# Performance work log

Measured on AMD Instinct MI355X. Metric: run time of the kernel, lower is better.

Reference implementation:

```python
import jax, jax.numpy as jnp
import numpy as np

N_P, N_A, N_S, D = 50000, 25000, 1, 64
ALPHA = 0.2  # leaky_relu negative slope
E_P2P, E_P2A, E_A2P, E_A2A = 800000, 400000, 400000, 400000


def _gat(z_msg, wh_dst, aw, src, dst, n_dst):
    """Per-edge-type GAT: score = leaky_relu(attn_fc([z_src ; Wh_dst])),
    segment softmax over destination, weighted scatter-sum of z_src.
    Attention linear is split into src/dst halves and applied per-node (cheaper)."""
    d = z_msg.shape[1]
    e = (z_msg @ aw[:d])[src] + (wh_dst @ aw[d:])[dst]  # [E]
    e = jnp.where(e > 0, e, ALPHA * e)                   # leaky_relu
    m = jax.ops.segment_max(e, dst, num_segments=n_dst)
    ex = jnp.exp(e - m[dst])
    den = jax.ops.segment_sum(ex, dst, num_segments=n_dst)
    w = ex / den[dst]                                    # per-dst softmax (mailbox softmax)
    return jax.ops.segment_sum(w[:, None] * z_msg[src], dst, num_segments=n_dst)


def setup_inputs() -> dict:
    ks = jax.random.split(jax.random.key(0), 32)
    sc = 1.0 / np.sqrt(D)
    f32, i32 = jnp.float32, jnp.int32
    inp = {
        "feat_P": jax.random.normal(ks[0], (N_P, D), f32),
        "feat_A": jax.random.normal(ks[1], (N_A, D), f32),
        "feat_state": jax.random.normal(ks[2], (N_S, D), f32),
    }
    for i, n in enumerate(["P", "A", "p2p", "p2a", "a2p", "a2a", "p2s", "a2s", "in"]):
        inp["W_" + n] = jax.random.normal(ks[3 + i], (D, D), f32) * sc
        inp["b_" + n] = jnp.zeros((D,), f32)
    for i, n in enumerate(["p2p", "p2a", "a2p", "a2a", "p2s", "a2s"]):
        inp["a_" + n] = jax.random.normal(ks[12 + i], (2 * D,), f32) * sc
    inp["src_p2p"] = jax.random.randint(ks[18], (E_P2P,), 0, N_P, i32)
    inp["dst_p2p"] = jax.random.randint(ks[19], (E_P2P,), 0, N_P, i32)
    inp["src_p2a"] = jax.random.randint(ks[20], (E_P2A,), 0, N_P, i32)
    inp["dst_p2a"] = jax.random.randint(ks[21], (E_P2A,), 0, N_A, i32)
    inp["src_a2p"] = jax.random.randint(ks[22], (E_A2P,), 0, N_A, i32)
    inp["dst_a2p"] = jax.random.randint(ks[23], (E_A2P,), 0, N_P, i32)
    inp["src_a2a"] = jax.random.randint(ks[24], (E_A2A,), 0, N_A, i32)
    inp["dst_a2a"] = jax.random.randint(ks[25], (E_A2A,), 0, N_A, i32)
    inp["src_p2s"] = jnp.arange(N_P, dtype=i32)
    inp["dst_p2s"] = jnp.zeros((N_P,), i32)
    inp["src_a2s"] = jnp.arange(N_A, dtype=i32)
    inp["dst_a2s"] = jnp.zeros((N_A,), i32)
    return inp


def reference(feat_P, feat_A, feat_state,
              W_P, b_P, W_A, b_A, W_p2p, b_p2p, W_p2a, b_p2a, W_a2p, b_a2p,
              W_a2a, b_a2a, W_p2s, b_p2s, W_a2s, b_a2s, W_in, b_in,
              a_p2p, a_p2a, a_a2p, a_a2a, a_p2s, a_a2s,
              src_p2p, dst_p2p, src_p2a, dst_p2a, src_a2p, dst_a2p,
              src_a2a, dst_a2a, src_p2s, dst_p2s, src_a2s, dst_a2s):
    Wh_P = feat_P @ W_P + b_P          # self transform per node type
    Wh_A = feat_A @ W_A + b_A
    Wh_in = feat_state @ W_in + b_in   # 'in' self-loop message to state
    h_P = jax.nn.relu(
        Wh_P
        + _gat(feat_P @ W_p2p + b_p2p, Wh_P, a_p2p, src_p2p, dst_p2p, N_P)
        + _gat(feat_A @ W_a2p + b_a2p, Wh_P, a_a2p, src_a2p, dst_a2p, N_P))
    h_A = jax.nn.relu(
        Wh_A
        + _gat(feat_P @ W_p2a + b_p2a, Wh_A, a_p2a, src_p2a, dst_p2a, N_A)
        + _gat(feat_A @ W_a2a + b_a2a, Wh_A, a_a2a, src_a2a, dst_a2a, N_A))
    h_S = jax.nn.relu(
        Wh_in
        + _gat(feat_P @ W_p2s + b_p2s, Wh_in, a_p2s, src_p2s, dst_p2s, N_S)
        + _gat(feat_A @ W_a2s + b_a2s, Wh_in, a_a2s, src_a2s, dst_a2s, N_S))
    return (h_P, h_A, h_S)
```

## Files before the change

kernel.cpp:

```cpp
#include <hip/hip_runtime.h>
#include <math.h>

#define ALPHA 0.2f
#define NP 50000
#define NA 25000
#define NBINS 150000
#define ABASE 100000
#define NBUCK 586
#define CH 4096
#define CAP 8192
#define GP ((NP + 63) / 64)
#define GA ((NA + 63) / 64)
#define SB_P 384
#define SB_A 192

typedef unsigned short u16;
typedef __attribute__((ext_vector_type(8))) short bf16x8;
typedef __attribute__((ext_vector_type(8))) unsigned short u16x8;
typedef __attribute__((ext_vector_type(4))) float f32x4;

__device__ __forceinline__ float bf2f(u16 u) { return __uint_as_float(((unsigned)u) << 16); }
__device__ __forceinline__ u16 f2bf(float f) {
    unsigned x = __float_as_uint(f);
    return (u16)((x + 0x7fffu + ((x >> 16) & 1u)) >> 16);
}

struct K1Args {
    const int *s0, *d0, *s1, *d1, *s2, *d2, *s3, *d3;
    int E0, E1, E2, E3, Etot, nblk;
    int *cursor0, *ebuf;
    const float *feat_P, *feat_A, *feat_S;
    const float *W_p2s, *b_p2s, *a_p2s, *W_a2s, *b_a2s, *a_a2s, *W_in, *b_in;
    float *numP, *numA, *den2;
};

struct K2Args {
    const int *ebuf; const int *cursor0;
    int *ssrc; int *offs;
    const float *feat_P, *feat_A, *feat_S;
    const float *W_P, *b_P, *W_A, *b_A, *W_p2p, *b_p2p, *W_p2a, *b_p2a,
                *W_a2p, *b_a2p, *W_a2a, *b_a2a, *W_p2s, *b_p2s, *W_a2s, *b_a2s,
                *W_in, *b_in;
    const float *a_p2p, *a_p2a, *a_a2p, *a_a2a;
    float *WhP, *WhA;
    u16 *z_p2p, *z_p2a, *z_a2p, *z_a2a;
    float *ss_p2p, *sd_p2p, *ss_p2a, *sd_p2a, *ss_a2p, *sd_a2p, *ss_a2a, *sd_a2a;
    const float *numP, *numA, *den2;
    float *outS;
};

__device__ __forceinline__ void edge_decode(int k,
    const int* __restrict__ s0, const int* __restrict__ d0, int E0,
    const int* __restrict__ s1, const int* __restrict__ d1, int E1,
    const int* __restrict__ s2, const int* __restrict__ d2, int E2,
    const int* __restrict__ s3, const int* __restrict__ d3,
    int& src, int& bin) {
    if (k < E0) { src = s0[k]; bin = 2 * d0[k]; return; }
    k -= E0; if (k < E1) { src = s1[k]; bin = 2 * d1[k] + 1; return; }
    k -= E1; if (k < E2) { src = s2[k]; bin = ABASE + 2 * d2[k]; return; }
    k -= E2; src = s3[k]; bin = ABASE + 2 * d3[k] + 1;
}

__global__ __launch_bounds__(256) void k1_kernel(K1Args A) {
    __shared__ int h[NBUCK];
    __shared__ int base[NBUCK];
    int bid = blockIdx.x;
    int tid = threadIdx.x;
    if (bid < A.nblk) {
        for (int i = tid; i < NBUCK; i += 256) h[i] = 0;
        __syncthreads();
        int b0 = bid * CH;
        int b1 = min(b0 + CH, A.Etot);
        int cbin[16], csrc[16];
#pragma unroll
        for (int it = 0; it < 16; ++it) {
            int i = b0 + it * 256 + tid;
            int bin = -1, src = 0;
            if (i < b1)
                edge_decode(i, A.s0, A.d0, A.E0, A.s1, A.d1, A.E1,
                            A.s2, A.d2, A.E2, A.s3, A.d3, src, bin);
            cbin[it] = bin; csrc[it] = src;
            if (bin >= 0) atomicAdd(&h[bin >> 8], 1);
        }
        __syncthreads();
        for (int i = tid; i < NBUCK; i += 256) {
            int c = h[i];
            base[i] = c ? (i * CAP + atomicAdd(&A.cursor0[i], c)) : 0;
            h[i] = 0;
        }
        __syncthreads();
#pragma unroll
        for (int it = 0; it < 16; ++it) {
            int bin = cbin[it];
            if (bin >= 0) {
                int bk = bin >> 8;
                int pos = base[bk] + atomicAdd(&h[bk], 1);
                if (pos < (bk + 1) * CAP)
                    A.ebuf[pos] = csrc[it] | ((bin & 255) << 16);
            }
        }
        return;
    }
    float* red = (float*)h;
    int sb = bid - A.nblk;
    bool isP = sb < SB_P;
    int bidl = isP ? sb : sb - SB_P;
    int nb = isP ? SB_P : SB_A;
    int N = isP ? NP : NA;
    const float* X   = isP ? A.feat_P : A.feat_A;
    const float* W   = isP ? A.W_p2s  : A.W_a2s;
    const float* b   = isP ? A.b_p2s  : A.b_a2s;
    const float* a   = isP ? A.a_p2s  : A.a_a2s;
    float* num       = isP ? A.numP   : A.numA;
    float* den       = isP ? &A.den2[0] : &A.den2[1];
    int lane = tid & 63, wv = tid >> 6;
    float v = 0.f;
    for (int c = 0; c < 64; ++c) v = fmaf(W[lane * 64 + c], a[c], v);
    float t0 = b[lane] * a[lane];
    float whc = A.b_in[lane];
    for (int k = 0; k < 64; ++k) whc = fmaf(A.feat_S[k], A.W_in[k * 64 + lane], whc);
    float t1 = whc * a[64 + lane];
#pragma unroll
    for (int o = 1; o < 64; o <<= 1) {
        t0 += __shfl_xor(t0, o, 64);
        t1 += __shfl_xor(t1, o, 64);
    }
    float cbias = t0 + t1;
    float accx = 0.f, accd = 0.f;
    int gw = bidl * 4 + wv, waves = nb * 4;
    for (int r = gw; r < N; r += waves) {
        float x = X[(long long)r * 64 + lane];
        float ss = x * v;
#pragma unroll
        for (int o = 1; o < 64; o <<= 1) ss += __shfl_xor(ss, o, 64);
        float e = ss + cbias;
        e = e > 0.f ? e : ALPHA * e;
        float w = __expf(e);
        accx = fmaf(w, x, accx);
        accd += w;
    }
    red[wv * 64 + lane] = accx;
    if (lane == 0) red[256 + wv] = accd;
    __syncthreads();
    if (tid < 64) {
        float t = red[tid] + red[64 + tid] + red[128 + tid] + red[192 + tid];
        atomicAdd(&num[tid], t);
    }
    if (tid == 64) atomicAdd(den, red[256] + red[257] + red[258] + red[259]);
}

__device__ void scan_counts(const int* __restrict__ counts, int* sstart) {
    __shared__ int wtot_sb[4];
    int tid = threadIdx.x, lane = tid & 63, wv = tid >> 6;
    int carry = 0;
    for (int c = 0; c < 3; ++c) {
        int i = c * 256 + tid;
        int v = (i < NBUCK) ? min(counts[i], CAP) : 0;
        int x = v;
#pragma unroll
        for (int o = 1; o < 64; o <<= 1) {
            int y = __shfl_up(x, o, 64);
            if (lane >= o) x += y;
        }
        if (lane == 63) wtot_sb[wv] = x;
        __syncthreads();
        int woff = carry;
        for (int j = 0; j < wv; ++j) woff += wtot_sb[j];
        int ctot = wtot_sb[0] + wtot_sb[1] + wtot_sb[2] + wtot_sb[3];
        if (i < NBUCK) sstart[i] = x + woff - v;
        __syncthreads();
        carry += ctot;
    }
    if (tid == 0) sstart[NBUCK] = carry;
    __syncthreads();
}

__device__ __forceinline__ void xform_body3(int bid,
    const float* __restrict__ X, int N,
    const float* __restrict__ W0, const float* __restrict__ b0, float* __restrict__ Wh,
    const float* __restrict__ dA, float* __restrict__ sdA,
    const float* __restrict__ dB, float* __restrict__ sdB,
    const float* __restrict__ W1, const float* __restrict__ b1, u16* __restrict__ z1,
    const float* __restrict__ v1, float* __restrict__ s1,
    const float* __restrict__ W2, const float* __restrict__ b2, u16* __restrict__ z2,
    const float* __restrict__ v2, float* __restrict__ s2)
{
    int tid = threadIdx.x, wv = tid >> 6, lane = tid & 63;
    if (wv == 3) return;
    int g = lane >> 4, li = lane & 15;
    const float* Wm = wv == 0 ? W0 : wv == 1 ? W1 : W2;
    const float* bm = wv == 0 ? b0 : wv == 1 ? b1 : b2;
    const float* dv = wv == 0 ? dA : wv == 1 ? v1 : v2;
    float* sm       = wv == 0 ? sdA : wv == 1 ? s1 : s2;
    u16* zm         = wv == 1 ? z1 : wv == 2 ? z2 : nullptr;

    bf16x8 Bf[4][2];
#pragma unroll
    for (int cb = 0; cb < 4; ++cb)
#pragma unroll
        for (int kc = 0; kc < 2; ++kc) {
            bf16x8 t;
#pragma unroll
            for (int j = 0; j < 8; ++j)
                t[j] = (short)f2bf(Wm[(kc * 32 + g * 8 + j) * 64 + cb * 16 + li]);
            Bf[cb][kc] = t;
        }
    float bl[4], dvl[4], dbl[4];
#pragma unroll
    for (int cb = 0; cb < 4; ++cb) {
        bl[cb]  = bm[cb * 16 + li];
        dvl[cb] = dv[cb * 16 + li];
        dbl[cb] = (wv == 0) ? dB[cb * 16 + li] : 0.f;
    }
    int base0 = bid * 64;
#pragma unroll
    for (int rt = 0; rt < 4; ++rt) {
        int rbase = base0 + rt * 16;
        if (rbase >= N) break;
        int rowC = min(rbase + li, N - 1);
        bf16x8 Af[2];
#pragma unroll
        for (int kc = 0; kc < 2; ++kc) {
            const float* xp = X + (long long)rowC * 64 + kc * 32 + g * 8;
            float4 x0 = *(const float4*)xp;
            float4 x1 = *(const float4*)(xp + 4);
            bf16x8 t;
            t[0] = (short)f2bf(x0.x); t[1] = (short)f2bf(x0.y);
            t[2] = (short)f2bf(x0.z); t[3] = (short)f2bf(x0.w);
            t[4] = (short)f2bf(x1.x); t[5] = (short)f2bf(x1.y);
            t[6] = (short)f2bf(x1.z); t[7] = (short)f2bf(x1.w);
            Af[kc] = t;
        }
        f32x4 acc[4] = {{0,0,0,0},{0,0,0,0},{0,0,0,0},{0,0,0,0}};
#pragma unroll
        for (int kc = 0; kc < 2; ++kc)
#pragma unroll
            for (int cb = 0; cb < 4; ++cb)
                acc[cb] = __builtin_amdgcn_mfma_f32_16x16x32_bf16(Af[kc], Bf[cb][kc], acc[cb], 0, 0, 0);
        float pd[4] = {0,0,0,0}, pb[4] = {0,0,0,0};
#pragma unroll
        for (int cb = 0; cb < 4; ++cb)
#pragma unroll
            for (int r = 0; r < 4; ++r) {
                float val = acc[cb][r] + bl[cb];
                acc[cb][r] = val;
                pd[r] = fmaf(val, dvl[cb], pd[r]);
                pb[r] = fmaf(val, dbl[cb], pb[r]);
            }
#pragma unroll
        for (int o = 1; o < 16; o <<= 1)
#pragma unroll
            for (int r = 0; r < 4; ++r) {
                pd[r] += __shfl_xor(pd[r], o, 64);
                pb[r] += __shfl_xor(pb[r], o, 64);
            }
        int rg = rbase + g * 4;
        if (li == 0) {
#pragma unroll
            for (int r = 0; r < 4; ++r) {
                int row = rg + r;
                if (row < N) {
                    sm[row] = pd[r];
                    if (wv == 0) sdB[row] = pb[r];
                }
            }
        }
        if (wv == 0) {
#pragma unroll
            for (int r = 0; r < 4; ++r) {
                int row = rg + r;
                if (row < N)
#pragma unroll
                    for (int cb = 0; cb < 4; ++cb)
                        Wh[(long long)row * 64 + cb * 16 + li] = acc[cb][r];
            }
        } else {
#pragma unroll
            for (int r = 0; r < 4; ++r) {
                int row = rg + r;
                if (row < N)
#pragma unroll
                    for (int cb = 0; cb < 4; ++cb)
                        zm[(long long)row * 64 + cb * 16 + li] = f2bf(acc[cb][r]);
            }
        }
    }
}

__global__ __launch_bounds__(256) void k2_kernel(K2Args A) {
    __shared__ int smem_i[NBUCK + 1 + 768 + 4];
    __shared__ u16 lsrc[CAP];
    int bid = blockIdx.x;
    int tid = threadIdx.x, lane = tid & 63, wv = tid >> 6;
    if (bid < NBUCK) {
        int* sstart = smem_i;
        int* lcnt = smem_i + NBUCK + 1;
        int* loff = lcnt + 256;
        int* lcur = loff + 256;
        int* wtot = lcur + 256;
        int b = bid;
        scan_counts(A.cursor0, sstart);
        int pstart = sstart[b];
        int rstart = b * CAP;
        int cnt = min(A.cursor0[b], CAP);
        lcnt[tid] = 0;
        __syncthreads();
        for (int e = tid; e < cnt; e += 256)
            atomicAdd(&lcnt[((unsigned)A.ebuf[rstart + e]) >> 16], 1);
        __syncthreads();
        int v = lcnt[tid];
        int x = v;
#pragma unroll
        for (int o = 1; o < 64; o <<= 1) {
            int y = __shfl_up(x, o, 64);
            if (lane >= o) x += y;
        }
        if (lane == 63) wtot[wv] = x;
        __syncthreads();
        int woff = 0;
        for (int j = 0; j < wv; ++j) woff += wtot[j];
        int excl = x + woff - v;
        loff[tid] = excl;
        lcur[tid] = excl;
        __syncthreads();
        for (int e = tid; e < cnt; e += 256) {
            int val = A.ebuf[rstart + e];
            int pos = atomicAdd(&lcur[((unsigned)val) >> 16], 1);
            lsrc[pos] = (u16)(val & 0xFFFF);
        }
        __syncthreads();
        for (int i = tid; i < cnt; i += 256) A.ssrc[pstart + i] = (int)lsrc[i];
        int gb = b * 256 + tid;
        if (gb < NBINS) A.offs[gb] = pstart + loff[tid];
        if (b == 0 && tid == 0) A.offs[NBINS] = sstart[NBUCK];
        return;
    }
    bid -= NBUCK;
    if (bid < GP) {
        xform_body3(bid, A.feat_P, NP,
                    A.W_P, A.b_P, A.WhP, A.a_p2p + 64, A.sd_p2p, A.a_a2p + 64, A.sd_a2p,
                    A.W_p2p, A.b_p2p, A.z_p2p, A.a_p2p, A.ss_p2p,
                    A.W_p2a, A.b_p2a, A.z_p2a, A.a_p2a, A.ss_p2a);
        return;
    }
    bid -= GP;
    if (bid < GA) {
        xform_body3(bid, A.feat_A, NA,
                    A.W_A, A.b_A, A.WhA, A.a_p2a + 64, A.sd_p2a, A.a_a2a + 64, A.sd_a2a,
                    A.W_a2p, A.b_a2p, A.z_a2p, A.a_a2p, A.ss_a2p,
                    A.W_a2a, A.b_a2a, A.z_a2a, A.a_a2a, A.ss_a2a);
        return;
    }
    if (tid < 64) {
        int c = tid;
        float whc = A.b_in[c];
        for (int k = 0; k < 64; ++k) whc = fmaf(A.feat_S[k], A.W_in[k * 64 + c], whc);
        float mp = 0.f, ma = 0.f;
        for (int k = 0; k < 64; ++k) {
            mp = fmaf(A.numP[k], A.W_p2s[k * 64 + c], mp);
            ma = fmaf(A.numA[k], A.W_a2s[k * 64 + c], ma);
        }
        float r = whc + mp / A.den2[0] + A.b_p2s[c] + ma / A.den2[1] + A.b_a2s[c];
        A.outS[c] = fmaxf(r, 0.f);
    }
}

__device__ __forceinline__ void seg_gat_g8(const int* __restrict__ ssrc, int s0, int s1,
                                           const float* __restrict__ ss, float sd,
                                           const u16* __restrict__ z, int lane,
                                           float* __restrict__ acc) {
    int cnt = s1 - s0;
    if (cnt <= 0) return;
    int egrp = lane >> 3, cg8 = (lane & 7) * 8;
    if (cnt <= 64) {
        int s = 0; float w = 0.f;
        if (lane < cnt) {
            s = ssrc[s0 + lane];
            float e = ss[s] + sd;
            e = e > 0.f ? e : ALPHA * e;
            w = __expf(e);
        }
        float den = w;
#pragma unroll
        for (int o = 32; o > 0; o >>= 1) den += __shfl_xor(den, o, 64);
        w *= 1.f / den;
        int nit = (cnt + 7) >> 3;
        for (int it = 0; it < nit; ++it) {
            int ei = it * 8 + egrp;
            float wt = __shfl(w, ei, 64);
            int   st = __shfl(s, ei, 64);
            u16x8 q = *(const u16x8*)(z + (long long)st * 64 + cg8);
#pragma unroll
            for (int j = 0; j < 8; ++j)
                acc[j] = fmaf(wt, bf2f(q[j]), acc[j]);
        }
    } else {
        float den = 0.f;
        for (int i = s0 + lane; i < s1; i += 64) {
            float e = ss[ssrc[i]] + sd; e = e > 0.f ? e : ALPHA * e; den += __expf(e);
        }
#pragma unroll
        for (int o = 32; o > 0; o >>= 1) den += __shfl_xor(den, o, 64);
        float inv = 1.f / den;
        for (int c = s0; c < s1; c += 64) {
            int i = c + lane; int s = 0; float w = 0.f;
            if (i < s1) {
                s = ssrc[i];
                float e = ss[s] + sd; e = e > 0.f ? e : ALPHA * e;
                w = __expf(e) * inv;
            }
            int cc = min(64, s1 - c);
            int nit = (cc + 7) >> 3;
            for (int it = 0; it < nit; ++it) {
                int ei = it * 8 + egrp;
                float wt = __shfl(w, ei, 64);
                int   st = __shfl(s, ei, 64);
                u16x8 q = *(const u16x8*)(z + (long long)st * 64 + cg8);
#pragma unroll
                for (int j = 0; j < 8; ++j)
                    acc[j] = fmaf(wt, bf2f(q[j]), acc[j]);
            }
        }
    }
}

__global__ __launch_bounds__(256) void gat_all(
    const int* __restrict__ ssrc, const int* __restrict__ offs,
    const float* __restrict__ WhP, float* __restrict__ outP,
    const float* __restrict__ WhA, float* __restrict__ outA,
    const float* __restrict__ ss_p2p, const float* __restrict__ sd_p2p, const u16* __restrict__ z_p2p,
    const float* __restrict__ ss_a2p, const float* __restrict__ sd_a2p, const u16* __restrict__ z_a2p,
    const float* __restrict__ ss_p2a, const float* __restrict__ sd_p2a, const u16* __restrict__ z_p2a,
    const float* __restrict__ ss_a2a, const float* __restrict__ sd_a2a, const u16* __restrict__ z_a2a) {
    int lane = threadIdx.x & 63;
    int g = (blockIdx.x * blockDim.x + threadIdx.x) >> 6;
    if (g >= NP + NA) return;
    bool isP = g < NP;
    int d = isP ? g : g - NP;
    int bin0 = isP ? 2 * d : ABASE + 2 * d;
    int e0 = offs[bin0], e1 = offs[bin0 + 1], e2 = offs[bin0 + 2];
    float acc[8] = {0.f, 0.f, 0.f, 0.f, 0.f, 0.f, 0.f, 0.f};
    if (isP) {
        seg_gat_g8(ssrc, e0, e1, ss_p2p, sd_p2p[d], z_p2p, lane, acc);
        seg_gat_g8(ssrc, e1, e2, ss_a2p, sd_a2p[d], z_a2p, lane, acc);
    } else {
        seg_gat_g8(ssrc, e0, e1, ss_p2a, sd_p2a[d], z_p2a, lane, acc);
        seg_gat_g8(ssrc, e1, e2, ss_a2a, sd_a2a[d], z_a2a, lane, acc);
    }
#pragma unroll
    for (int o = 8; o <= 32; o <<= 1)
#pragma unroll
        for (int j = 0; j < 8; ++j)
            acc[j] += __shfl_xor(acc[j], o, 64);
    if (lane < 8) {
        const float* Wh = isP ? WhP : WhA;
        float* outp = isP ? outP : outA;
        const float* sp = &Wh[(long long)d * 64 + lane * 8];
        float4 s0v = *(const float4*)sp;
        float4 s1v = *(const float4*)(sp + 4);
        float4 r0, r1;
        r0.x = fmaxf(s0v.x + acc[0], 0.f); r0.y = fmaxf(s0v.y + acc[1], 0.f);
        r0.z = fmaxf(s0v.z + acc[2], 0.f); r0.w = fmaxf(s0v.w + acc[3], 0.f);
        r1.x = fmaxf(s1v.x + acc[4], 0.f); r1.y = fmaxf(s1v.y + acc[5], 0.f);
        r1.z = fmaxf(s1v.z + acc[6], 0.f); r1.w = fmaxf(s1v.w + acc[7], 0.f);
        float* op = &outp[(long long)d * 64 + lane * 8];
        *(float4*)op = r0;
        *(float4*)(op + 4) = r1;
    }
}

extern "C" void kernel_launch(void* const* d_in, const int* in_sizes, int n_in,
                              void* d_out, int out_size, void* d_ws, size_t ws_size,
                              hipStream_t stream) {
    const float* feat_P = (const float*)d_in[0];
    const float* feat_A = (const float*)d_in[1];
    const float* feat_S = (const float*)d_in[2];
    const float* W_P   = (const float*)d_in[3];  const float* b_P   = (const float*)d_in[4];
    const float* W_A   = (const float*)d_in[5];  const float* b_A   = (const float*)d_in[6];
    const float* W_p2p = (const float*)d_in[7];  const float* b_p2p = (const float*)d_in[8];
    const float* W_p2a = (const float*)d_in[9];  const float* b_p2a = (const float*)d_in[10];
    const float* W_a2p = (const float*)d_in[11]; const float* b_a2p = (const float*)d_in[12];
    const float* W_a2a = (const float*)d_in[13]; const float* b_a2a = (const float*)d_in[14];
    const float* W_p2s = (const float*)d_in[15]; const float* b_p2s = (const float*)d_in[16];
    const float* W_a2s = (const float*)d_in[17]; const float* b_a2s = (const float*)d_in[18];
    const float* W_in  = (const float*)d_in[19]; const float* b_in  = (const float*)d_in[20];
    const float* a_p2p = (const float*)d_in[21];
    const float* a_p2a = (const float*)d_in[22];
    const float* a_a2p = (const float*)d_in[23];
    const float* a_a2a = (const float*)d_in[24];
    const float* a_p2s = (const float*)d_in[25];
    const float* a_a2s = (const float*)d_in[26];
    const int* src_p2p = (const int*)d_in[27]; const int* dst_p2p = (const int*)d_in[28];
    const int* src_p2a = (const int*)d_in[29]; const int* dst_p2a = (const int*)d_in[30];
    const int* src_a2p = (const int*)d_in[31]; const int* dst_a2p = (const int*)d_in[32];
    const int* src_a2a = (const int*)d_in[33]; const int* dst_a2a = (const int*)d_in[34];
    int E_p2p = in_sizes[27], E_p2a = in_sizes[29], E_a2p = in_sizes[31], E_a2a = in_sizes[33];
    int E_tot = E_p2p + E_a2p + E_p2a + E_a2a;

    float* out = (float*)d_out;
    float* outP = out;
    float* outA = out + (long long)NP * 64;
    float* outS = out + (long long)(NP + NA) * 64;

    float* ws = (float*)d_ws;
    float* WhP = ws; ws += (long long)NP * 64;
    float* WhA = ws; ws += (long long)NA * 64;
    u16* z_p2p = (u16*)ws; ws += (long long)NP * 32;
    u16* z_p2a = (u16*)ws; ws += (long long)NP * 32;
    u16* z_a2p = (u16*)ws; ws += (long long)NA * 32;
    u16* z_a2a = (u16*)ws; ws += (long long)NA * 32;
    float* ss_p2p = ws; ws += NP;  float* sd_p2p = ws; ws += NP;
    float* ss_p2a = ws; ws += NP;  float* sd_p2a = ws; ws += NA;
    float* ss_a2p = ws; ws += NA;  float* sd_a2p = ws; ws += NP;
    float* ss_a2a = ws; ws += NA;  float* sd_a2a = ws; ws += NA;
    float* zreg = ws;
    int*   cursor0 = (int*)ws; ws += NBUCK;
    float* den2 = ws; ws += 2;
    float* numP = ws; ws += 64;
    float* numA = ws; ws += 64;
    size_t zbytes = (size_t)((char*)ws - (char*)zreg);
    int* iw = (int*)ws;
    int* ebuf = iw; iw += NBUCK * CAP;
    int* ssrc = iw; iw += E_tot;
    int* offs = iw; iw += NBINS + 1;

    const int T = 256;
    int nblk = (E_tot + CH - 1) / CH;

    hipMemsetAsync(zreg, 0, zbytes, stream);

    K1Args K1;
    K1.s0 = src_p2p; K1.d0 = dst_p2p; K1.s1 = src_a2p; K1.d1 = dst_a2p;
    K1.s2 = src_p2a; K1.d2 = dst_p2a; K1.s3 = src_a2a; K1.d3 = dst_a2a;
    K1.E0 = E_p2p; K1.E1 = E_a2p; K1.E2 = E_p2a; K1.E3 = E_a2a;
    K1.Etot = E_tot; K1.nblk = nblk;
    K1.cursor0 = cursor0; K1.ebuf = ebuf;
    K1.feat_P = feat_P; K1.feat_A = feat_A; K1.feat_S = feat_S;
    K1.W_p2s = W_p2s; K1.b_p2s = b_p2s; K1.a_p2s = a_p2s;
    K1.W_a2s = W_a2s; K1.b_a2s = b_a2s; K1.a_a2s = a_a2s;
    K1.W_in = W_in; K1.b_in = b_in;
    K1.numP = numP; K1.numA = numA; K1.den2 = den2;
    k1_kernel<<<nblk + SB_P + SB_A, T, 0, stream>>>(K1);

    K2Args K2;
    K2.ebuf = ebuf; K2.cursor0 = cursor0; K2.ssrc = ssrc; K2.offs = offs;
    K2.feat_P = feat_P; K2.feat_A = feat_A; K2.feat_S = feat_S;
    K2.W_P = W_P; K2.b_P = b_P; K2.W_A = W_A; K2.b_A = b_A;
    K2.W_p2p = W_p2p; K2.b_p2p = b_p2p; K2.W_p2a = W_p2a; K2.b_p2a = b_p2a;
    K2.W_a2p = W_a2p; K2.b_a2p = b_a2p; K2.W_a2a = W_a2a; K2.b_a2a = b_a2a;
    K2.W_p2s = W_p2s; K2.b_p2s = b_p2s; K2.W_a2s = W_a2s; K2.b_a2s = b_a2s;
    K2.W_in = W_in; K2.b_in = b_in;
    K2.a_p2p = a_p2p; K2.a_p2a = a_p2a; K2.a_a2p = a_a2p; K2.a_a2a = a_a2a;
    K2.WhP = WhP; K2.WhA = WhA;
    K2.z_p2p = z_p2p; K2.z_p2a = z_p2a; K2.z_a2p = z_a2p; K2.z_a2a = z_a2a;
    K2.ss_p2p = ss_p2p; K2.sd_p2p = sd_p2p; K2.ss_p2a = ss_p2a; K2.sd_p2a = sd_p2a;
    K2.ss_a2p = ss_a2p; K2.sd_a2p = sd_a2p; K2.ss_a2a = ss_a2a; K2.sd_a2a = sd_a2a;
    K2.numP = numP; K2.numA = numA; K2.den2 = den2; K2.outS = outS;
    k2_kernel<<<NBUCK + GP + GA + 1, T, 0, stream>>>(K2);

    gat_all<<<((NP + NA) * 64 + T - 1) / T, T, 0, stream>>>(ssrc, offs,
        WhP, outP, WhA, outA,
        ss_p2p, sd_p2p, z_p2p, ss_a2p, sd_a2p, z_a2p,
        ss_p2a, sd_p2a, z_p2a, ss_a2a, sd_a2a, z_a2a);
}
```

Baseline: 131.6 us.

## Move node transforms into the edge-bucketing kernel and store sorted sources as u16

The per-node MFMA transforms (Wh, z, and the attention src/dst scores) move out of k2 and into k1, where they run alongside the edge bucketing and state-reduction blocks. Each wave now handles one (matrix, row-block) item, so the previously idle fourth wave of every block does work, and k2 keeps only the sort/scan and the state output. The sorted source index array is narrowed from int to u16, which halves its write and read traffic in k2 and gat_all. The cost is a larger, more varied k1 grid. The u16 sources rely on node indices being below 65536.

```diff
diff --git a/kernel.cpp b/kernel.cpp
--- a/kernel.cpp
+++ b/kernel.cpp
@@ -11,6 +11,9 @@
 #define CAP 8192
 #define GP ((NP + 63) / 64)
 #define GA ((NA + 63) / 64)
+#define XWI_P (3 * GP)
+#define XWI (3 * GP + 3 * GA)
+#define XWB ((XWI + 3) / 4)
 #define SB_P 384
 #define SB_A 192
 
@@ -30,21 +33,21 @@
     int E0, E1, E2, E3, Etot, nblk;
     int *cursor0, *ebuf;
     const float *feat_P, *feat_A, *feat_S;
-    const float *W_p2s, *b_p2s, *a_p2s, *W_a2s, *b_a2s, *a_a2s, *W_in, *b_in;
-    float *numP, *numA, *den2;
-};
-
-struct K2Args {
-    const int *ebuf; const int *cursor0;
-    int *ssrc; int *offs;
-    const float *feat_P, *feat_A, *feat_S;
     const float *W_P, *b_P, *W_A, *b_A, *W_p2p, *b_p2p, *W_p2a, *b_p2a,
-                *W_a2p, *b_a2p, *W_a2a, *b_a2a, *W_p2s, *b_p2s, *W_a2s, *b_a2s,
-                *W_in, *b_in;
+                *W_a2p, *b_a2p, *W_a2a, *b_a2a;
     const float *a_p2p, *a_p2a, *a_a2p, *a_a2a;
     float *WhP, *WhA;
     u16 *z_p2p, *z_p2a, *z_a2p, *z_a2a;
     float *ss_p2p, *sd_p2p, *ss_p2a, *sd_p2a, *ss_a2p, *sd_a2p, *ss_a2a, *sd_a2a;
+    const float *W_p2s, *b_p2s, *a_p2s, *W_a2s, *b_a2s, *a_a2s, *W_in, *b_in;
+    float *numP, *numA, *den2;
+};
+
+struct K2Args {
+    const int *ebuf; const int *cursor0;
+    u16 *ssrc; int *offs;
+    const float *feat_S;
+    const float *W_p2s, *b_p2s, *W_a2s, *b_a2s, *W_in, *b_in;
     const float *numP, *numA, *den2;
     float *outS;
 };
@@ -61,139 +64,15 @@
     k -= E2; src = s3[k]; bin = ABASE + 2 * d3[k] + 1;
 }
 
-__global__ __launch_bounds__(256) void k1_kernel(K1Args A) {
-    __shared__ int h[NBUCK];
-    __shared__ int base[NBUCK];
-    int bid = blockIdx.x;
-    int tid = threadIdx.x;
-    if (bid < A.nblk) {
-        for (int i = tid; i < NBUCK; i += 256) h[i] = 0;
-        __syncthreads();
-        int b0 = bid * CH;
-        int b1 = min(b0 + CH, A.Etot);
-        int cbin[16], csrc[16];
-#pragma unroll
-        for (int it = 0; it < 16; ++it) {
-            int i = b0 + it * 256 + tid;
-            int bin = -1, src = 0;
-            if (i < b1)
-                edge_decode(i, A.s0, A.d0, A.E0, A.s1, A.d1, A.E1,
-                            A.s2, A.d2, A.E2, A.s3, A.d3, src, bin);
-            cbin[it] = bin; csrc[it] = src;
-            if (bin >= 0) atomicAdd(&h[bin >> 8], 1);
-        }
-        __syncthreads();
-        for (int i = tid; i < NBUCK; i += 256) {
-            int c = h[i];
-            base[i] = c ? (i * CAP + atomicAdd(&A.cursor0[i], c)) : 0;
-            h[i] = 0;
-        }
-        __syncthreads();
-#pragma unroll
-        for (int it = 0; it < 16; ++it) {
-            int bin = cbin[it];
-            if (bin >= 0) {
-                int bk = bin >> 8;
-                int pos = base[bk] + atomicAdd(&h[bk], 1);
-                if (pos < (bk + 1) * CAP)
-                    A.ebuf[pos] = csrc[it] | ((bin & 255) << 16);
-            }
-        }
-        return;
-    }
-    float* red = (float*)h;
-    int sb = bid - A.nblk;
-    bool isP = sb < SB_P;
-    int bidl = isP ? sb : sb - SB_P;
-    int nb = isP ? SB_P : SB_A;
-    int N = isP ? NP : NA;
-    const float* X   = isP ? A.feat_P : A.feat_A;
-    const float* W   = isP ? A.W_p2s  : A.W_a2s;
-    const float* b   = isP ? A.b_p2s  : A.b_a2s;
-    const float* a   = isP ? A.a_p2s  : A.a_a2s;
-    float* num       = isP ? A.numP   : A.numA;
-    float* den       = isP ? &A.den2[0] : &A.den2[1];
-    int lane = tid & 63, wv = tid >> 6;
-    float v = 0.f;
-    for (int c = 0; c < 64; ++c) v = fmaf(W[lane * 64 + c], a[c], v);
-    float t0 = b[lane] * a[lane];
-    float whc = A.b_in[lane];
-    for (int k = 0; k < 64; ++k) whc = fmaf(A.feat_S[k], A.W_in[k * 64 + lane], whc);
-    float t1 = whc * a[64 + lane];
-#pragma unroll
-    for (int o = 1; o < 64; o <<= 1) {
-        t0 += __shfl_xor(t0, o, 64);
-        t1 += __shfl_xor(t1, o, 64);
-    }
-    float cbias = t0 + t1;
-    float accx = 0.f, accd = 0.f;
-    int gw = bidl * 4 + wv, waves = nb * 4;
-    for (int r = gw; r < N; r += waves) {
-        float x = X[(long long)r * 64 + lane];
-        float ss = x * v;
-#pragma unroll
-        for (int o = 1; o < 64; o <<= 1) ss += __shfl_xor(ss, o, 64);
-        float e = ss + cbias;
-        e = e > 0.f ? e : ALPHA * e;
-        float w = __expf(e);
-        accx = fmaf(w, x, accx);
-        accd += w;
-    }
-    red[wv * 64 + lane] = accx;
-    if (lane == 0) red[256 + wv] = accd;
-    __syncthreads();
-    if (tid < 64) {
-        float t = red[tid] + red[64 + tid] + red[128 + tid] + red[192 + tid];
-        atomicAdd(&num[tid], t);
-    }
-    if (tid == 64) atomicAdd(den, red[256] + red[257] + red[258] + red[259]);
-}
-
-__device__ void scan_counts(const int* __restrict__ counts, int* sstart) {
-    __shared__ int wtot_sb[4];
-    int tid = threadIdx.x, lane = tid & 63, wv = tid >> 6;
-    int carry = 0;
-    for (int c = 0; c < 3; ++c) {
-        int i = c * 256 + tid;
-        int v = (i < NBUCK) ? min(counts[i], CAP) : 0;
-        int x = v;
-#pragma unroll
-        for (int o = 1; o < 64; o <<= 1) {
-            int y = __shfl_up(x, o, 64);
-            if (lane >= o) x += y;
-        }
-        if (lane == 63) wtot_sb[wv] = x;
-        __syncthreads();
-        int woff = carry;
-        for (int j = 0; j < wv; ++j) woff += wtot_sb[j];
-        int ctot = wtot_sb[0] + wtot_sb[1] + wtot_sb[2] + wtot_sb[3];
-        if (i < NBUCK) sstart[i] = x + woff - v;
-        __syncthreads();
-        carry += ctot;
-    }
-    if (tid == 0) sstart[NBUCK] = carry;
-    __syncthreads();
-}
-
-__device__ __forceinline__ void xform_body3(int bid,
+__device__ __forceinline__ void xform_item(int rb,
     const float* __restrict__ X, int N,
-    const float* __restrict__ W0, const float* __restrict__ b0, float* __restrict__ Wh,
-    const float* __restrict__ dA, float* __restrict__ sdA,
+    const float* __restrict__ Wm, const float* __restrict__ bm,
+    const float* __restrict__ dv, float* __restrict__ sm,
     const float* __restrict__ dB, float* __restrict__ sdB,
-    const float* __restrict__ W1, const float* __restrict__ b1, u16* __restrict__ z1,
-    const float* __restrict__ v1, float* __restrict__ s1,
-    const float* __restrict__ W2, const float* __restrict__ b2, u16* __restrict__ z2,
-    const float* __restrict__ v2, float* __restrict__ s2)
+    float* __restrict__ whout, u16* __restrict__ zm,
+    int lane)
 {
-    int tid = threadIdx.x, wv = tid >> 6, lane = tid & 63;
-    if (wv == 3) return;
     int g = lane >> 4, li = lane & 15;
-    const float* Wm = wv == 0 ? W0 : wv == 1 ? W1 : W2;
-    const float* bm = wv == 0 ? b0 : wv == 1 ? b1 : b2;
-    const float* dv = wv == 0 ? dA : wv == 1 ? v1 : v2;
-    float* sm       = wv == 0 ? sdA : wv == 1 ? s1 : s2;
-    u16* zm         = wv == 1 ? z1 : wv == 2 ? z2 : nullptr;
-
     bf16x8 Bf[4][2];
 #pragma unroll
     for (int cb = 0; cb < 4; ++cb)
@@ -210,9 +89,9 @@
     for (int cb = 0; cb < 4; ++cb) {
         bl[cb]  = bm[cb * 16 + li];
         dvl[cb] = dv[cb * 16 + li];
-        dbl[cb] = (wv == 0) ? dB[cb * 16 + li] : 0.f;
-    }
-    int base0 = bid * 64;
+        dbl[cb] = sdB ? dB[cb * 16 + li] : 0.f;
+    }
+    int base0 = rb * 64;
 #pragma unroll
     for (int rt = 0; rt < 4; ++rt) {
         int rbase = base0 + rt * 16;
@@ -261,18 +140,18 @@
                 int row = rg + r;
                 if (row < N) {
                     sm[row] = pd[r];
-                    if (wv == 0) sdB[row] = pb[r];
+                    if (sdB) sdB[row] = pb[r];
                 }
             }
         }
-        if (wv == 0) {
+        if (whout) {
 #pragma unroll
             for (int r = 0; r < 4; ++r) {
                 int row = rg + r;
                 if (row < N)
 #pragma unroll
                     for (int cb = 0; cb < 4; ++cb)
-                        Wh[(long long)row * 64 + cb * 16 + li] = acc[cb][r];
+                        whout[(long long)row * 64 + cb * 16 + li] = acc[cb][r];
             }
         } else {
 #pragma unroll
@@ -285,6 +164,146 @@
             }
         }
     }
+}
+
+__global__ __launch_bounds__(256) void k1_kernel(K1Args A) {
+    __shared__ int h[NBUCK];
+    __shared__ int base[NBUCK];
+    int bid = blockIdx.x;
+    int tid = threadIdx.x, lane = tid & 63, wv = tid >> 6;
+    if (bid < A.nblk) {
+        for (int i = tid; i < NBUCK; i += 256) h[i] = 0;
+        __syncthreads();
+        int b0 = bid * CH;
+        int b1 = min(b0 + CH, A.Etot);
+        int cbin[16], csrc[16];
+#pragma unroll
+        for (int it = 0; it < 16; ++it) {
+            int i = b0 + it * 256 + tid;
+            int bin = -1, src = 0;
+            if (i < b1)
+                edge_decode(i, A.s0, A.d0, A.E0, A.s1, A.d1, A.E1,
+                            A.s2, A.d2, A.E2, A.s3, A.d3, src, bin);
+            cbin[it] = bin; csrc[it] = src;
+            if (bin >= 0) atomicAdd(&h[bin >> 8], 1);
+        }
+        __syncthreads();
+        for (int i = tid; i < NBUCK; i += 256) {
+            int c = h[i];
+            base[i] = c ? (i * CAP + atomicAdd(&A.cursor0[i], c)) : 0;
+            h[i] = 0;
+        }
+        __syncthreads();
+#pragma unroll
+        for (int it = 0; it < 16; ++it) {
+            int bin = cbin[it];
+            if (bin >= 0) {
+                int bk = bin >> 8;
+                int pos = base[bk] + atomicAdd(&h[bk], 1);
+                if (pos < (bk + 1) * CAP)
+                    A.ebuf[pos] = csrc[it] | ((bin & 255) << 16);
+            }
+        }
+        return;
+    }
+    bid -= A.nblk;
+    if (bid < XWB) {
+        int item = bid * 4 + wv;
+        if (item >= XWI) return;
+        bool isP = item < XWI_P;
+        int m, rb;
+        if (isP) { m = item / GP; rb = item % GP; }
+        else     { int it2 = item - XWI_P; m = it2 / GA; rb = it2 % GA; }
+        const float* X = isP ? A.feat_P : A.feat_A;
+        int N = isP ? NP : NA;
+        const float *Wm, *bm, *dv, *dB = nullptr;
+        float *sm, *sdB = nullptr, *whout = nullptr;
+        u16 *zm = nullptr;
+        if (isP) {
+            if (m == 0)      { Wm = A.W_P;   bm = A.b_P;   dv = A.a_p2p + 64; sm = A.sd_p2p;
+                               dB = A.a_a2p + 64; sdB = A.sd_a2p; whout = A.WhP; }
+            else if (m == 1) { Wm = A.W_p2p; bm = A.b_p2p; dv = A.a_p2p; sm = A.ss_p2p; zm = A.z_p2p; }
+            else             { Wm = A.W_p2a; bm = A.b_p2a; dv = A.a_p2a; sm = A.ss_p2a; zm = A.z_p2a; }
+        } else {
+            if (m == 0)      { Wm = A.W_A;   bm = A.b_A;   dv = A.a_p2a + 64; sm = A.sd_p2a;
+                               dB = A.a_a2a + 64; sdB = A.sd_a2a; whout = A.WhA; }
+            else if (m == 1) { Wm = A.W_a2p; bm = A.b_a2p; dv = A.a_a2p; sm = A.ss_a2p; zm = A.z_a2p; }
+            else             { Wm = A.W_a2a; bm = A.b_a2a; dv = A.a_a2a; sm = A.ss_a2a; zm = A.z_a2a; }
+        }
+        xform_item(rb, X, N, Wm, bm, dv, sm, dB, sdB, whout, zm, lane);
+        return;
+    }
+    bid -= XWB;
+    float* red = (float*)h;
+    bool isP = bid < SB_P;
+    int bidl = isP ? bid : bid - SB_P;
+    int nb = isP ? SB_P : SB_A;
+    int N = isP ? NP : NA;
+    const float* X   = isP ? A.feat_P : A.feat_A;
+    const float* W   = isP ? A.W_p2s  : A.W_a2s;
+    const float* b   = isP ? A.b_p2s  : A.b_a2s;
+    const float* a   = isP ? A.a_p2s  : A.a_a2s;
+    float* num       = isP ? A.numP   : A.numA;
+    float* den       = isP ? &A.den2[0] : &A.den2[1];
+    float v = 0.f;
+    for (int c = 0; c < 64; ++c) v = fmaf(W[lane * 64 + c], a[c], v);
+    float t0 = b[lane] * a[lane];
+    float whc = A.b_in[lane];
+    for (int k = 0; k < 64; ++k) whc = fmaf(A.feat_S[k], A.W_in[k * 64 + lane], whc);
+    float t1 = whc * a[64 + lane];
+#pragma unroll
+    for (int o = 1; o < 64; o <<= 1) {
+        t0 += __shfl_xor(t0, o, 64);
+        t1 += __shfl_xor(t1, o, 64);
+    }
+    float cbias = t0 + t1;
+    float accx = 0.f, accd = 0.f;
+    int gw = bidl * 4 + wv, waves = nb * 4;
+    for (int r = gw; r < N; r += waves) {
+        float x = X[(long long)r * 64 + lane];
+        float ss = x * v;
+#pragma unroll
+        for (int o = 1; o < 64; o <<= 1) ss += __shfl_xor(ss, o, 64);
+        float e = ss + cbias;
+        e = e > 0.f ? e : ALPHA * e;
+        float w = __expf(e);
+        accx = fmaf(w, x, accx);
+        accd += w;
+    }
+    red[wv * 64 + lane] = accx;
+    if (lane == 0) red[256 + wv] = accd;
+    __syncthreads();
+    if (tid < 64) {
+        float t = red[tid] + red[64 + tid] + red[128 + tid] + red[192 + tid];
+        atomicAdd(&num[tid], t);
+    }
+    if (tid == 64) atomicAdd(den, red[256] + red[257] + red[258] + red[259]);
+}
+
+__device__ void scan_counts(const int* __restrict__ counts, int* sstart) {
+    __shared__ int wtot_sb[4];
+    int tid = threadIdx.x, lane = tid & 63, wv = tid >> 6;
+    int carry = 0;
+    for (int c = 0; c < 3; ++c) {
+        int i = c * 256 + tid;
+        int v = (i < NBUCK) ? min(counts[i], CAP) : 0;
+        int x = v;
+#pragma unroll
+        for (int o = 1; o < 64; o <<= 1) {
+            int y = __shfl_up(x, o, 64);
+            if (lane >= o) x += y;
+        }
+        if (lane == 63) wtot_sb[wv] = x;
+        __syncthreads();
+        int woff = carry;
+        for (int j = 0; j < wv; ++j) woff += wtot_sb[j];
+        int ctot = wtot_sb[0] + wtot_sb[1] + wtot_sb[2] + wtot_sb[3];
+        if (i < NBUCK) sstart[i] = x + woff - v;
+        __syncthreads();
+        carry += ctot;
+    }
+    if (tid == 0) sstart[NBUCK] = carry;
+    __syncthreads();
 }
 
 __global__ __launch_bounds__(256) void k2_kernel(K2Args A) {
@@ -329,26 +348,10 @@
             lsrc[pos] = (u16)(val & 0xFFFF);
         }
         __syncthreads();
-        for (int i = tid; i < cnt; i += 256) A.ssrc[pstart + i] = (int)lsrc[i];
+        for (int i = tid; i < cnt; i += 256) A.ssrc[pstart + i] = lsrc[i];
         int gb = b * 256 + tid;
         if (gb < NBINS) A.offs[gb] = pstart + loff[tid];
         if (b == 0 && tid == 0) A.offs[NBINS] = sstart[NBUCK];
-        return;
-    }
-    bid -= NBUCK;
-    if (bid < GP) {
-        xform_body3(bid, A.feat_P, NP,
-                    A.W_P, A.b_P, A.WhP, A.a_p2p + 64, A.sd_p2p, A.a_a2p + 64, A.sd_a2p,
-                    A.W_p2p, A.b_p2p, A.z_p2p, A.a_p2p, A.ss_p2p,
-                    A.W_p2a, A.b_p2a, A.z_p2a, A.a_p2a, A.ss_p2a);
-        return;
-    }
-    bid -= GP;
-    if (bid < GA) {
-        xform_body3(bid, A.feat_A, NA,
-                    A.W_A, A.b_A, A.WhA, A.a_p2a + 64, A.sd_p2a, A.a_a2a + 64, A.sd_a2a,
-                    A.W_a2p, A.b_a2p, A.z_a2p, A.a_a2p, A.ss_a2p,
-                    A.W_a2a, A.b_a2a, A.z_a2a, A.a_a2a, A.ss_a2a);
         return;
     }
     if (tid < 64) {
@@ -365,7 +368,7 @@
     }
 }
 
-__device__ __forceinline__ void seg_gat_g8(const int* __restrict__ ssrc, int s0, int s1,
+__device__ __forceinline__ void seg_gat_g8(const u16* __restrict__ ssrc, int s0, int s1,
                                            const float* __restrict__ ss, float sd,
                                            const u16* __restrict__ z, int lane,
                                            float* __restrict__ acc) {
@@ -375,7 +378,7 @@
     if (cnt <= 64) {
         int s = 0; float w = 0.f;
         if (lane < cnt) {
-            s = ssrc[s0 + lane];
+            s = (int)ssrc[s0 + lane];
             float e = ss[s] + sd;
             e = e > 0.f ? e : ALPHA * e;
             w = __expf(e);
@@ -397,7 +400,7 @@
     } else {
         float den = 0.f;
         for (int i = s0 + lane; i < s1; i += 64) {
-            float e = ss[ssrc[i]] + sd; e = e > 0.f ? e : ALPHA * e; den += __expf(e);
+            float e = ss[(int)ssrc[i]] + sd; e = e > 0.f ? e : ALPHA * e; den += __expf(e);
         }
 #pragma unroll
         for (int o = 32; o > 0; o >>= 1) den += __shfl_xor(den, o, 64);
@@ -405,7 +408,7 @@
         for (int c = s0; c < s1; c += 64) {
             int i = c + lane; int s = 0; float w = 0.f;
             if (i < s1) {
-                s = ssrc[i];
+                s = (int)ssrc[i];
                 float e = ss[s] + sd; e = e > 0.f ? e : ALPHA * e;
                 w = __expf(e) * inv;
             }
@@ -425,7 +428,7 @@
 }
 
 __global__ __launch_bounds__(256) void gat_all(
-    const int* __restrict__ ssrc, const int* __restrict__ offs,
+    const u16* __restrict__ ssrc, const int* __restrict__ offs,
     const float* __restrict__ WhP, float* __restrict__ outP,
     const float* __restrict__ WhA, float* __restrict__ outA,
     const float* __restrict__ ss_p2p, const float* __restrict__ sd_p2p, const u16* __restrict__ z_p2p,
@@ -521,7 +524,7 @@
     size_t zbytes = (size_t)((char*)ws - (char*)zreg);
     int* iw = (int*)ws;
     int* ebuf = iw; iw += NBUCK * CAP;
-    int* ssrc = iw; iw += E_tot;
+    u16* ssrc = (u16*)iw; iw += (E_tot + 1) / 2;
     int* offs = iw; iw += NBINS + 1;
 
     const int T = 256;
@@ -536,27 +539,27 @@
     K1.Etot = E_tot; K1.nblk = nblk;
     K1.cursor0 = cursor0; K1.ebuf = ebuf;
     K1.feat_P = feat_P; K1.feat_A = feat_A; K1.feat_S = feat_S;
+    K1.W_P = W_P; K1.b_P = b_P; K1.W_A = W_A; K1.b_A = b_A;
+    K1.W_p2p = W_p2p; K1.b_p2p = b_p2p; K1.W_p2a = W_p2a; K1.b_p2a = b_p2a;
+    K1.W_a2p = W_a2p; K1.b_a2p = b_a2p; K1.W_a2a = W_a2a; K1.b_a2a = b_a2a;
+    K1.a_p2p = a_p2p; K1.a_p2a = a_p2a; K1.a_a2p = a_a2p; K1.a_a2a = a_a2a;
+    K1.WhP = WhP; K1.WhA = WhA;
+    K1.z_p2p = z_p2p; K1.z_p2a = z_p2a; K1.z_a2p = z_a2p; K1.z_a2a = z_a2a;
+    K1.ss_p2p = ss_p2p; K1.sd_p2p = sd_p2p; K1.ss_p2a = ss_p2a; K1.sd_p2a = sd_p2a;
+    K1.ss_a2p = ss_a2p; K1.sd_a2p = sd_a2p; K1.ss_a2a = ss_a2a; K1.sd_a2a = sd_a2a;
     K1.W_p2s = W_p2s; K1.b_p2s = b_p2s; K1.a_p2s = a_p2s;
     K1.W_a2s = W_a2s; K1.b_a2s = b_a2s; K1.a_a2s = a_a2s;
     K1.W_in = W_in; K1.b_in = b_in;
     K1.numP = numP; K1.numA = numA; K1.den2 = den2;
-    k1_kernel<<<nblk + SB_P + SB_A, T, 0, stream>>>(K1);
+    k1_kernel<<<nblk + XWB + SB_P + SB_A, T, 0, stream>>>(K1);
 
     K2Args K2;
     K2.ebuf = ebuf; K2.cursor0 = cursor0; K2.ssrc = ssrc; K2.offs = offs;
-    K2.feat_P = feat_P; K2.feat_A = feat_A; K2.feat_S = feat_S;
-    K2.W_P = W_P; K2.b_P = b_P; K2.W_A = W_A; K2.b_A = b_A;
-    K2.W_p2p = W_p2p; K2.b_p2p = b_p2p; K2.W_p2a = W_p2a; K2.b_p2a = b_p2a;
-    K2.W_a2p = W_a2p; K2.b_a2p = b_a2p; K2.W_a2a = W_a2a; K2.b_a2a = b_a2a;
+    K2.feat_S = feat_S;
     K2.W_p2s = W_p2s; K2.b_p2s = b_p2s; K2.W_a2s = W_a2s; K2.b_a2s = b_a2s;
     K2.W_in = W_in; K2.b_in = b_in;
-    K2.a_p2p = a_p2p; K2.a_p2a = a_p2a; K2.a_a2p = a_a2p; K2.a_a2a = a_a2a;
-    K2.WhP = WhP; K2.WhA = WhA;
-    K2.z_p2p = z_p2p; K2.z_p2a = z_p2a; K2.z_a2p = z_a2p; K2.z_a2a = z_a2a;
-    K2.ss_p2p = ss_p2p; K2.sd_p2p = sd_p2p; K2.ss_p2a = ss_p2a; K2.sd_p2a = sd_p2a;
-    K2.ss_a2p = ss_a2p; K2.sd_a2p = sd_a2p; K2.ss_a2a = ss_a2a; K2.sd_a2a = sd_a2a;
     K2.numP = numP; K2.numA = numA; K2.den2 = den2; K2.outS = outS;
-    k2_kernel<<<NBUCK + GP + GA + 1, T, 0, stream>>>(K2);
+    k2_kernel<<<NBUCK + 1, T, 0, stream>>>(K2);
 
     gat_all<<<((NP + NA) * 64 + T - 1) / T, T, 0, stream>>>(ssrc, offs,
         WhP, outP, WhA, outA,
```

Measured after the change: 140.1 us. 6.5% more time.
